# Kernel optimization log

Measured on AMD Instinct MI355X. Metric: run time of the kernel, lower is better.

The kernel has to match this reference:

```python
import jax, jax.numpy as jnp
import numpy as np

E = 512   # embed_size == hidden_size (required: step-0 'embed' is the init output of size hidden)
H = 512
A = 512   # attention dim
V = 20000
P = 196
B = 128
T = 24


def setup_inputs() -> dict:
    key = jax.random.key(0)
    ks = jax.random.split(key, 20)
    s = 0.02
    return {
        "features": jax.random.normal(ks[0], (B, P, E), jnp.float32),
        "captions": jax.random.randint(ks[1], (B, T), 0, V),
        "emb": jax.random.normal(ks[2], (V, E), jnp.float32) * s,
        "W_init_h": jax.random.normal(ks[3], (E, H), jnp.float32) * s,
        "b_init_h": jnp.zeros((H,), jnp.float32),
        "W_init_o": jax.random.normal(ks[4], (E, H), jnp.float32) * s,
        "b_init_o": jnp.zeros((H,), jnp.float32),
        "Wf": jax.random.normal(ks[5], (E, A), jnp.float32) * s,
        "bf": jnp.zeros((A,), jnp.float32),
        "Wh": jax.random.normal(ks[6], (H, A), jnp.float32) * s,
        "bh": jnp.zeros((A,), jnp.float32),
        "v_att": jax.random.normal(ks[7], (A,), jnp.float32) * s,
        "W_ih": jax.random.normal(ks[8], (3 * H, 2 * E), jnp.float32) * s,
        "W_hh": jax.random.normal(ks[9], (3 * H, H), jnp.float32) * s,
        "b_ih": jnp.zeros((3 * H,), jnp.float32),
        "b_hh": jnp.zeros((3 * H,), jnp.float32),
        "W_out": jax.random.normal(ks[10], (V, H), jnp.float32) * s,
        "b_out": jnp.zeros((V,), jnp.float32),
    }


def reference(features, emb, W_init_h, b_init_h, W_init_o, b_init_o,
              Wf, bf, Wh, bh, v_att, W_ih, W_hh, b_ih, b_hh,
              W_out, b_out, captions):
    # init_hidden_state
    avg = features.mean(axis=1)                          # [B,E]
    hidden0 = jnp.tanh(avg @ W_init_h + b_init_h)        # [B,H]
    output0 = jnp.tanh(avg @ W_init_o + b_init_o)        # [B,H]

    emb_caps = emb[captions]                             # [B,T,E]
    # teacher forcing: step 0 uses init output, step i>0 uses embeddings[:, i-1]
    embed_seq = jnp.concatenate([output0[:, None, :], emb_caps[:, :-1, :]], axis=1)
    xs = embed_seq.transpose(1, 0, 2)                    # [T,B,E]

    feat_proj = features @ Wf + bf                       # [B,P,A] (precompute attn key proj)

    def step(h, x_emb):
        # additive attention over pixels
        score = jnp.tanh(feat_proj + (h @ Wh + bh)[:, None, :]) @ v_att   # [B,P]
        alpha = jax.nn.softmax(score, axis=1)
        ctx = jnp.einsum('bp,bpe->be', alpha, features)                   # [B,E]
        x = jnp.concatenate([x_emb, ctx], axis=1)                         # [B,2E]
        # single-step GRU (PyTorch gate order r,z,n)
        gi = x @ W_ih.T + b_ih
        gh = h @ W_hh.T + b_hh
        gi_r, gi_z, gi_n = jnp.split(gi, 3, axis=1)
        gh_r, gh_z, gh_n = jnp.split(gh, 3, axis=1)
        r = jax.nn.sigmoid(gi_r + gh_r)
        z = jax.nn.sigmoid(gi_z + gh_z)
        n = jnp.tanh(gi_n + r * gh_n)
        h_new = (1.0 - z) * n + z * h
        pred = h_new @ W_out.T + b_out                                    # [B,V]
        return h_new, pred

    _, preds = jax.lax.scan(step, hidden0, xs)           # preds: [T,B,V]
    return preds.transpose(1, 0, 2)                      # [B,T,V]
```

## Files before the change

### kernel.cpp

```cpp
#include <hip/hip_runtime.h>

#define Bb 128
#define Tt 24
#define Ee 512
#define Hh 512
#define Aa 512
#define Vv 20000
#define Pp 196
#define TV (Tt*Vv)
#define NBLK 512
#define NTHR 256
#define GT (NBLK*NTHR)
#define SMEM_BYTES 34816

typedef __attribute__((ext_vector_type(8))) short bfrag;
typedef __attribute__((ext_vector_type(4))) float f4;
typedef __attribute__((ext_vector_type(4))) unsigned short us4;

#define MFMA16(a,b,c) __builtin_amdgcn_mfma_f32_16x16x32_bf16(a,b,c,0,0,0)

__device__ __forceinline__ unsigned short f2bf(float f){
  unsigned int x = __builtin_bit_cast(unsigned int, f);
  x += 0x7fffu + ((x >> 16) & 1u);
  return (unsigned short)(x >> 16);
}
__device__ __forceinline__ float bfu2f(unsigned short u){
  unsigned int x = ((unsigned int)u) << 16;
  return __builtin_bit_cast(float, x);
}
#define LOG2E 1.442695041f
__device__ __forceinline__ float fexp2(float x){ return __builtin_amdgcn_exp2f(x); }
__device__ __forceinline__ float frcp (float x){ return __builtin_amdgcn_rcpf(x); }
__device__ __forceinline__ float tanh_f(float x){ return 1.0f - 2.0f*frcp(1.0f + fexp2((2.0f*LOG2E)*x)); }
__device__ __forceinline__ float sigm_f(float x){ return frcp(1.0f + fexp2(-LOG2E*x)); }

__device__ __forceinline__ unsigned long long scld8(const void* p){
  return __hip_atomic_load((const unsigned long long*)p, __ATOMIC_RELAXED, __HIP_MEMORY_SCOPE_AGENT);
}
__device__ __forceinline__ unsigned scld4(const unsigned* p){
  return __hip_atomic_load(p, __ATOMIC_RELAXED, __HIP_MEMORY_SCOPE_AGENT);
}
__device__ __forceinline__ void scst4(unsigned* p, unsigned v){
  __hip_atomic_store(p, v, __ATOMIC_RELAXED, __HIP_MEMORY_SCOPE_AGENT);
}
__device__ __forceinline__ void scstf(float* p, float v){
  __hip_atomic_store(p, v, __ATOMIC_RELAXED, __HIP_MEMORY_SCOPE_AGENT);
}

__device__ __forceinline__ void set_flag(unsigned* line, unsigned v){
  asm volatile("s_waitcnt vmcnt(0)" ::: "memory");
  __syncthreads();
  if(threadIdx.x == 0) scst4(line, v);
}
__device__ __forceinline__ void poll_flags(const unsigned* base, int n, unsigned tgt){
  int tid = threadIdx.x;
  for(;;){
    int ok = (tid < n) ? (scld4(base + tid*16) >= tgt) : 1;
    if(__syncthreads_count(ok) == NTHR) break;
    __builtin_amdgcn_s_sleep(4);
  }
  asm volatile("" ::: "memory");
}

__device__ __forceinline__ void gbar2(unsigned* sync, unsigned phase){
  __syncthreads();
  int tid = threadIdx.x, blk = blockIdx.x;
  if(tid == 0)
    (void)__hip_atomic_fetch_add(sync + (blk & 31)*16, 1u,
                                 __ATOMIC_RELEASE, __HIP_MEMORY_SCOPE_AGENT);
  if(blk == 0){
    for(;;){
      int ok = (tid < 32) ? (scld4(sync + tid*16) >= phase*16u) : 1;
      if(__syncthreads_count(ok) == NTHR) break;
      __builtin_amdgcn_s_sleep(2);
    }
    if(tid == 0) scst4(sync + 32*16, phase);
  }
  if(tid == 0){
    while(scld4(sync + 32*16) < phase) __builtin_amdgcn_s_sleep(2);
    (void)__hip_atomic_load(sync + 32*16, __ATOMIC_ACQUIRE, __HIP_MEMORY_SCOPE_AGENT);
  }
  __syncthreads();
}

__global__ void k_zero(unsigned* s){
  int i = blockIdx.x*256 + threadIdx.x;
  s[i] = 0u;
}

__device__ __forceinline__ void cast_loop(const float* __restrict__ s,
                                          unsigned short* __restrict__ d,
                                          int n4, int gtid){
  for(int i = gtid; i < n4; i += GT){
    float4 v = ((const float4*)s)[i];
    us4 o; o[0]=f2bf(v.x); o[1]=f2bf(v.y); o[2]=f2bf(v.z); o[3]=f2bf(v.w);
    ((us4*)d)[i] = o;
  }
}
__device__ __forceinline__ void tr_tile(const float* __restrict__ S,
                                        unsigned short* __restrict__ D,
                                        int it, int jt, int tid, float (*T)[33]){
  int er = tid>>3, c4 = (tid&7)*4;
  float4 v = *(const float4*)(S + (size_t)(jt*32+er)*512 + it*32 + c4);
  T[er][c4+0]=v.x; T[er][c4+1]=v.y; T[er][c4+2]=v.z; T[er][c4+3]=v.w;
  __syncthreads();
  us4 o;
  o[0]=f2bf(T[c4+0][er]); o[1]=f2bf(T[c4+1][er]);
  o[2]=f2bf(T[c4+2][er]); o[3]=f2bf(T[c4+3][er]);
  *(us4*)(D + (size_t)(it*32+er)*512 + jt*32 + c4) = o;
  __syncthreads();
}

__device__ __forceinline__ void stage16(char* dstSM, const unsigned short* src, int R0){
  int tid = threadIdx.x;
  #pragma unroll
  for(int j=0;j<8;j++){
    int u = tid + j*256;
    int row = u >> 7, c8 = u & 127;
    unsigned long long q = scld8(src + (size_t)(R0+row)*Hh + c8*4);
    int bo = (row<<10) + (c8<<3);
    bo ^= (row&7)<<4;
    *(unsigned long long*)(dstSM + bo) = q;
  }
}


__device__ void attention_task(int b, const float* __restrict__ hpr_t,
                               const unsigned short* __restrict__ fpb,
                               const unsigned short* __restrict__ featsB,
                               const float* __restrict__ vatt,
                               unsigned short* __restrict__ ctx_t, char* SM)
{
  float* hp  = (float*)SM;
  float* vp  = hp + 512;
  float* sc  = vp + 512;
  float* red = sc + 200;
  int tid = threadIdx.x;
  {
    unsigned long long q = scld8(hpr_t + (size_t)b*Aa + tid*2);
    float2 hv = __builtin_bit_cast(float2, q);
    float2 vv = *(const float2*)(vatt + tid*2);
    int a0 = tid*2, a1 = a0+1;
    hp[((a0&31)<<4)+(a0>>5)] = hv.x;
    hp[((a1&31)<<4)+(a1>>5)] = hv.y;
    vp[((a0&31)<<4)+(a0>>5)] = vv.x;
    vp[((a1&31)<<4)+(a1>>5)] = vv.y;
  }
  __syncthreads();
  int grp = tid >> 4, gl = tid & 15;
  for(int pass=0; pass<13; pass++){
    int p = pass*16 + grp;
    float acc = 0.0f;
    if(p < Pp){
      const unsigned short* fr = fpb + ((size_t)b*Pp + p)*Aa + gl*32;
      #pragma unroll
      for(int j=0;j<32;j+=8){
        bfrag fv = *(const bfrag*)(fr + j);
        #pragma unroll
        for(int q=0;q<8;q++){
          int idx = ((j+q)<<4) + gl;
          float x = bfu2f((unsigned short)fv[q]) + hp[idx];
          acc += tanh_f(x) * vp[idx];
        }
      }
    }
    acc += __shfl_xor(acc, 1, 64);
    acc += __shfl_xor(acc, 2, 64);
    acc += __shfl_xor(acc, 4, 64);
    acc += __shfl_xor(acc, 8, 64);
    if(p < Pp && gl == 0) sc[p] = acc;
  }
  __syncthreads();
  if(tid < 64){
    float m = -1e30f;
    for(int i=0;i<4;i++){ int p = tid + i*64; if(p < Pp) m = fmaxf(m, sc[p]); }
    for(int off=1; off<64; off<<=1) m = fmaxf(m, __shfl_xor(m, off, 64));
    float s = 0.0f;
    for(int i=0;i<4;i++){ int p = tid + i*64; if(p < Pp) s += fexp2((sc[p]-m)*LOG2E); }
    for(int off=1; off<64; off<<=1) s += __shfl_xor(s, off, 64);
    if(tid == 0){ red[0] = m; red[1] = frcp(s); }
  }
  __syncthreads();
  float mx = red[0], rS = red[1];
  float al_t = 0.0f;
  if(tid < Pp) al_t = fexp2((sc[tid]-mx)*LOG2E) * rS;
  __syncthreads();
  if(tid < Pp) sc[tid] = al_t;
  __syncthreads();
  float c0 = 0.f, c1 = 0.f;
  const unsigned int* fb = (const unsigned int*)(featsB + (size_t)b*Pp*Ee);
  for(int p=0;p<Pp;p++){
    float al = sc[p];
    unsigned int u = fb[(size_t)p*256 + tid];
    unsigned int lo = (u & 0xffffu) << 16, hi = u & 0xffff0000u;
    c0 += al * __builtin_bit_cast(float, lo);
    c1 += al * __builtin_bit_cast(float, hi);
  }
  unsigned int cw = ((unsigned int)f2bf(c1) << 16) | (unsigned int)f2bf(c0);
  scst4((unsigned*)ctx_t + (size_t)b*256 + tid, cw);
}

__device__ void hproj_mfma(int R0, int HC0, const char* SMh,
                           const unsigned short* __restrict__ WhT,
                           const float* __restrict__ bhv, float* __restrict__ hpr)
{
  int tid = threadIdx.x;
  int w = tid>>6, l = tid&63, l16 = l&15, lk = l>>4;
  int a = HC0 + w*16 + l16;
  f4 acc = (f4)(0.0f);
  for(int k0=0;k0<512;k0+=32){
    int koff = k0 + lk*8;
    int bo = (l16<<10) + (koff<<1); bo ^= (l16&7)<<4;
    bfrag ah = *(const bfrag*)(SMh + bo);
    bfrag bq = *(const bfrag*)(WhT + (size_t)a*Hh + koff);
    acc = MFMA16(ah, bq, acc);
  }
  float bias = bhv[a];
  #pragma unroll
  for(int i=0;i<4;i++){
    int row = lk*4 + i;
    scstf(hpr + (size_t)(R0+row)*Aa + a, acc[i] + bias);
  }
}

__device__ void gates_phaseA(int R0, int HC0, const unsigned short* __restrict__ eseqT,
                             const unsigned short* __restrict__ WihB,
                             const unsigned short* __restrict__ WhhB,
                             const char* SMh, f4 (&agh)[3], f4 (&agi)[3])
{
  int tid = threadIdx.x;
  int w = tid>>6, l = tid&63, l16 = l&15, lk = l>>4;
  int hcol = HC0 + w*16 + l16;
  #pragma unroll
  for(int q=0;q<3;q++){ agh[q]=(f4)(0.f); agi[q]=(f4)(0.f); }
  for(int k0=0;k0<512;k0+=32){
    int koff = k0 + lk*8;
    int bo = (l16<<10) + (koff<<1); bo ^= (l16&7)<<4;
    bfrag ah = *(const bfrag*)(SMh + bo);
    bfrag ae = *(const bfrag*)(eseqT + (size_t)(R0+l16)*Ee + koff);
    #pragma unroll
    for(int q=0;q<3;q++){
      int j = q*512 + hcol;
      bfrag bh_ = *(const bfrag*)(WhhB + (size_t)j*512  + koff);
      bfrag be  = *(const bfrag*)(WihB + (size_t)j*1024 + koff);
      agh[q] = MFMA16(ah, bh_, agh[q]);
      agi[q] = MFMA16(ae, be,  agi[q]);
    }
  }
}

__device__ void gates_phaseB(int R0, int HC0, const char* SMc,
                             const unsigned short* __restrict__ WihB,
                             const float* __restrict__ bih, const float* __restrict__ bhh,
                             const float* __restrict__ hf_cur, float* __restrict__ hf_nxt,
                             unsigned short* __restrict__ hbU_nxt,
                             f4 (&agh)[3], f4 (&agi)[3], char* SM_HB)
{
  int tid = threadIdx.x;
  int w = tid>>6, l = tid&63, l16 = l&15, lk = l>>4;
  int hcol = HC0 + w*16 + l16;
  for(int k0=0;k0<512;k0+=32){
    int koff = k0 + lk*8;
    int bo = (l16<<10) + (koff<<1); bo ^= (l16&7)<<4;
    bfrag ac = *(const bfrag*)(SMc + bo);
    #pragma unroll
    for(int q=0;q<3;q++){
      int j = q*512 + hcol;
      bfrag bc = *(const bfrag*)(WihB + (size_t)j*1024 + 512 + koff);
      agi[q] = MFMA16(ac, bc, agi[q]);
    }
  }
  float bir = bih[hcol],      bhr = bhh[hcol];
  float biz = bih[512+hcol],  bhz = bhh[512+hcol];
  float bin = bih[1024+hcol], bhn = bhh[1024+hcol];
  unsigned short (*HB)[64] = (unsigned short(*)[64])SM_HB;
  #pragma unroll
  for(int i=0;i<4;i++){
    int row = lk*4 + i;
    int b = R0 + row;
    float r_ = sigm_f(agi[0][i] + bir + agh[0][i] + bhr);
    float z_ = sigm_f(agi[1][i] + biz + agh[1][i] + bhz);
    float n_ = tanh_f(agi[2][i] + bin + r_*(agh[2][i] + bhn));
    float ho = hf_cur[(size_t)b*Hh + hcol];
    float hn = (1.0f - z_)*n_ + z_*ho;
    hf_nxt[(size_t)b*Hh + hcol] = hn;
    HB[row][w*16 + l16] = f2bf(hn);
  }
  __syncthreads();
  #pragma unroll
  for(int j=0;j<2;j++){
    int widx = tid + j*256;
    int row = widx >> 5, pr = widx & 31;
    unsigned uu = (unsigned)HB[row][pr*2] | ((unsigned)HB[row][pr*2+1] << 16);
    scst4((unsigned*)(hbU_nxt + (size_t)(R0+row)*Hh + HC0) + pr, uu);
  }
}

__device__ void pred_task32(int pt, int tw, const unsigned short* __restrict__ hb_cur,
                            const unsigned short* __restrict__ WoutB,
                            const float* __restrict__ bout, float* __restrict__ out,
                            char* SM)
{
  int tid = threadIdx.x;
  int vchunk = pt >> 2, mbase = (pt & 3)*32;
  #pragma unroll
  for(int j=0;j<16;j++){
    int u = tid + j*256;
    int row = u >> 7, c8 = u & 127;
    unsigned long long q = scld8(hb_cur + (size_t)(mbase+row)*Hh + c8*4);
    int bo = (row<<10) + (c8<<3);
    bo ^= (row&7)<<4;
    *(unsigned long long*)(SM + bo) = q;
  }
  __syncthreads();
  int w = tid>>6, l = tid&63, l16 = l&15, lk = l>>4;
  int nb = vchunk*256 + w*64;
  f4 acc[2][4];
  #pragma unroll
  for(int mi=0;mi<2;mi++) for(int ni=0;ni<4;ni++) acc[mi][ni] = (f4)(0.0f);
  for(int k0=0;k0<512;k0+=32){
    int koff = k0 + lk*8;
    bfrag af[2], bq[4];
    #pragma unroll
    for(int mi=0;mi<2;mi++){
      int row = mi*16 + l16;
      int bo = (row<<10) + (koff<<1);
      bo ^= (row&7)<<4;
      af[mi] = *(const bfrag*)(SM + bo);
    }
    #pragma unroll
    for(int ni=0;ni<4;ni++){
      int v = nb + ni*16 + l16; if(v > Vv-1) v = Vv-1;
      bq[ni] = *(const bfrag*)(WoutB + (size_t)v*Hh + koff);
    }
    #pragma unroll
    for(int mi=0;mi<2;mi++)
      #pragma unroll
      for(int ni=0;ni<4;ni++)
        acc[mi][ni] = MFMA16(af[mi], bq[ni], acc[mi][ni]);
  }
  #pragma unroll
  for(int ni=0;ni<4;ni++){
    int v = nb + ni*16 + l16;
    if(v < Vv){
      float bias = bout[v];
      #pragma unroll
      for(int mi=0;mi<2;mi++){
        #pragma unroll
        for(int i=0;i<4;i++){
          int br = mbase + mi*16 + lk*4 + i;
          __builtin_nontemporal_store(acc[mi][ni][i] + bias,
              out + (size_t)br*TV + (size_t)tw*Vv + v);
        }
      }
    }
  }
  __syncthreads();
}

__global__ __launch_bounds__(NTHR, 4) void k_all(
    const float* feats, const int* caps, const float* emb,
    const float* Winh, const float* binh, const float* Wino, const float* bino,
    const float* Wf, const float* bfv, const float* Wh, const float* bhv,
    const float* vatt, const float* Wih, const float* Whh,
    const float* bih, const float* bhh, const float* Wout, const float* bout,
    float* out,
    float* hfR, unsigned short* hbU, float* hpr,
    unsigned short* ctxR, unsigned short* avgB, unsigned short* eseq,
    unsigned short* WfT, unsigned short* WhT,
    unsigned short* WinhT, unsigned short* WinoT,
    unsigned short* WihB, unsigned short* WhhB,
    unsigned short* fpb, unsigned short* featsB, unsigned short* WoutB,
    unsigned* sync)
{
  extern __shared__ char SMEM[];
  const int blk = blockIdx.x, tid = threadIdx.x;
  const int gtid = blk*NTHR + tid;
  unsigned* flagsA = sync + 40*16;
  unsigned* flagsG = sync + 168*16;
  unsigned* flagsP = sync + 240*16;
  unsigned* aggP   = sync + 304*16;
  float* h_f0 = hfR;
  unsigned short* h_b0 = hbU;

  cast_loop(Wih,  WihB,  (3*Hh*2*Ee)/4, gtid);
  cast_loop(Whh,  WhhB,  (3*Hh*Hh)/4,   gtid);
  cast_loop(Wout, WoutB, (Vv*Hh)/4,     gtid);
  cast_loop(feats,featsB,(Bb*Pp*Ee)/4,  gtid);
  for(int task = blk; task < 1024; task += NBLK){
    int z = task >> 8, rt = task & 255;
    int it = rt & 15, jt = rt >> 4;
    const float* S = (z==0)?Wf:(z==1)?Wh:(z==2)?Winh:Wino;
    unsigned short* D = (z==0)?WfT:(z==1)?WhT:(z==2)?WinhT:WinoT;
    tr_tile(S, D, it, jt, tid, (float(*)[33])SMEM);
  }
  if(blk < Bb){
    int b = blk;
    const float* fb = feats + (size_t)b*Pp*Ee;
    float a0=0.f, a1=0.f;
    for(int p=0;p<Pp;p++){
      float2 v = *(const float2*)(fb + (size_t)p*Ee + tid*2);
      a0 += v.x; a1 += v.y;
    }
    a0 *= (1.0f/Pp); a1 *= (1.0f/Pp);
    unsigned int pack = ((unsigned int)f2bf(a1)<<16) | (unsigned int)f2bf(a0);
    ((unsigned int*)avgB)[(size_t)b*256 + tid] = pack;
  }
  for(int task = blk; task < (Tt-1)*Bb; task += NBLK){
    int ts = task/Bb + 1, b = task%Bb;
    int cap = caps[b*Tt + (ts-1)];
    float2 v = *(const float2*)(emb + (size_t)cap*Ee + tid*2);
    unsigned int pack = ((unsigned int)f2bf(v.y)<<16) | (unsigned int)f2bf(v.x);
    ((unsigned int*)(eseq + ((size_t)ts*Bb + b)*Ee))[tid] = pack;
  }
  gbar2(sync, 1);

  for(int task = blk; task < 1584; task += NBLK){
    int w = tid>>6, l = tid&63, l16 = l&15, lk = l>>4;
    if(task < 1568){
      int bx = task % 196, by = task / 196;
      size_t m_base = (size_t)bx*128 + (w&1)*64;
      int nb = by*64 + (w>>1)*32;
      f4 acc[4][2];
      #pragma unroll
      for(int mi=0;mi<4;mi++) for(int ni=0;ni<2;ni++) acc[mi][ni] = (f4)(0.0f);
      for(int k0=0;k0<512;k0+=32){
        int koff = k0 + lk*8;
        bfrag af[4], bq[2];
        #pragma unroll
        for(int mi=0;mi<4;mi++) af[mi] = *(const bfrag*)(featsB + (m_base+mi*16+l16)*512 + koff);
        #pragma unroll
        for(int ni=0;ni<2;ni++) bq[ni] = *(const bfrag*)(WfT + (size_t)(nb+ni*16+l16)*512 + koff);
        #pragma unroll
        for(int mi=0;mi<4;mi++)
          #pragma unroll
          for(int ni=0;ni<2;ni++)
            acc[mi][ni] = MFMA16(af[mi], bq[ni], acc[mi][ni]);
      }
      #pragma unroll
      for(int ni=0;ni<2;ni++){
        int a = nb + ni*16 + l16;
        float bias = bfv[a];
        #pragma unroll
        for(int mi=0;mi<4;mi++){
          size_t r = m_base + mi*16 + lk*4;
          #pragma unroll
          for(int i=0;i<4;i++)
            fpb[(r+i)*512 + a] = f2bf(acc[mi][ni][i] + bias);
        }
      }
    } else {
      int idx = task - 1568;
      int y = idx >> 3, xb = idx & 7;
      int m0 = (w&1)*64, nb = xb*64 + (w>>1)*32;
      const unsigned short* Wt = y ? WinoT : WinhT;
      const float* bias = y ? bino : binh;
      f4 acc[4][2];
      #pragma unroll
      for(int mi=0;mi<4;mi++) for(int ni=0;ni<2;ni++) acc[mi][ni] = (f4)(0.0f);
      for(int k0=0;k0<512;k0+=32){
        int koff = k0 + lk*8;
        bfrag af[4], bq[2];
        #pragma unroll
        for(int mi=0;mi<4;mi++) af[mi] = *(const bfrag*)(avgB + (size_t)(m0+mi*16+l16)*512 + koff);
        #pragma unroll
        for(int ni=0;ni<2;ni++) bq[ni] = *(const bfrag*)(Wt + (size_t)(nb+ni*16+l16)*512 + koff);
        #pragma unroll
        for(int mi=0;mi<4;mi++)
          #pragma unroll
          for(int ni=0;ni<2;ni++)
            acc[mi][ni] = MFMA16(af[mi], bq[ni], acc[mi][ni]);
      }
      #pragma unroll
      for(int ni=0;ni<2;ni++){
        int n = nb + ni*16 + l16;
        float bv = bias[n];
        #pragma unroll
        for(int mi=0;mi<4;mi++){
          int bb = m0 + mi*16 + lk*4;
          #pragma unroll
          for(int i=0;i<4;i++){
            float val = tanh_f(acc[mi][ni][i] + bv);
            if(y==0){ h_f0[(size_t)(bb+i)*Hh + n] = val; h_b0[(size_t)(bb+i)*Hh + n] = f2bf(val); }
            else    { eseq[(size_t)(bb+i)*Ee + n] = f2bf(val); }
          }
        }
      }
    }
  }
  gbar2(sync, 2);

  int xcd = blk & 7, slot = blk >> 3;

  if(slot < 16){
    int b = slot*8 + xcd;
    int rg = b >> 4;
    for(int t=0; t<Tt; t++){
      poll_flags(flagsP + rg*8*16, 8, (unsigned)(t+1));
      attention_task(b, hpr + (size_t)(t&1)*Bb*Aa, fpb, featsB, vatt,
                     ctxR + (size_t)(t&3)*Bb*Ee, SMEM);
      set_flag(flagsA + b*16, (unsigned)(t+1));
    }
  } else if(slot < 24){
    int r = slot - 16, c = xcd;
    int R0 = r*16, HC0 = c*64;
    char* SMh = SMEM;
    char* SMc = SMEM + 16384;
    char* SMB = SMEM + 32768;
    f4 agh[3], agi[3];
    stage16(SMh, hbU, R0);
    __syncthreads();
    hproj_mfma(R0, HC0, SMh, WhT, bhv, hpr);
    set_flag(flagsP + (r*8+c)*16, 1u);
    gates_phaseA(R0, HC0, eseq, WihB, WhhB, SMh, agh, agi);
    for(int t=0; t<Tt; t++){
      poll_flags(flagsA + R0*16, 16, (unsigned)(t+1));
      stage16(SMc, ctxR + (size_t)(t&3)*Bb*Ee, R0);
      __syncthreads();
      gates_phaseB(R0, HC0, SMc, WihB, bih, bhh,
                   hfR + (size_t)(t&1)*Bb*Hh, hfR + (size_t)((t+1)&1)*Bb*Hh,
                   hbU + (size_t)(t+1)*Bb*Hh, agh, agi, SMB);
      set_flag(flagsG + (r*8+c)*16, (unsigned)(t+1));
      if(t+1 < Tt){
        poll_flags(flagsG + r*8*16, 8, (unsigned)(t+1));
        stage16(SMh, hbU + (size_t)(t+1)*Bb*Hh, R0);
        __syncthreads();
        hproj_mfma(R0, HC0, SMh, WhT, bhv, hpr + (size_t)((t+1)&1)*Bb*Aa);
        set_flag(flagsP + (r*8+c)*16, (unsigned)(t+2));
        gates_phaseA(R0, HC0, eseq + (size_t)(t+1)*Bb*Ee, WihB, WhhB, SMh, agh, agi);
      }
    }
  } else {
    int ps = slot - 24;
    int pt = xcd*40 + ps;
    if(ps == 0){
      for(int t=1; t<=Tt; t++){
        poll_flags(flagsG, 64, (unsigned)t);
        if(tid == 0) scst4(aggP + xcd*16, (unsigned)t);
        pred_task32(pt, t-1, hbU + (size_t)t*Bb*Hh, WoutB, bout, out, SMEM);
      }
    } else if(pt < 316){
      for(int t=1; t<=Tt; t++){
        poll_flags(aggP + xcd*16, 1, (unsigned)t);
        pred_task32(pt, t-1, hbU + (size_t)t*Bb*Hh, WoutB, bout, out, SMEM);
      }
    }
  }
}

extern "C" void kernel_launch(void* const* d_in, const int* in_sizes, int n_in,
                              void* d_out, int out_size, void* d_ws, size_t ws_size,
                              hipStream_t stream)
{
  const float* feats = (const float*)d_in[0];
  const int*   caps  = (const int*)d_in[1];
  const float* emb   = (const float*)d_in[2];
  const float* Winh  = (const float*)d_in[3];
  const float* binh  = (const float*)d_in[4];
  const float* Wino  = (const float*)d_in[5];
  const float* bino  = (const float*)d_in[6];
  const float* Wf    = (const float*)d_in[7];
  const float* bfv   = (const float*)d_in[8];
  const float* Wh    = (const float*)d_in[9];
  const float* bhv   = (const float*)d_in[10];
  const float* vatt  = (const float*)d_in[11];
  const float* Wih   = (const float*)d_in[12];
  const float* Whh   = (const float*)d_in[13];
  const float* bih   = (const float*)d_in[14];
  const float* bhh   = (const float*)d_in[15];
  const float* Wout  = (const float*)d_in[16];
  const float* bout  = (const float*)d_in[17];
  float* out = (float*)d_out;

  char* ws = (char*)d_ws;
  size_t off = 0;
  auto alloc = [&](size_t bytes){
    off = (off + 255) & ~(size_t)255;
    void* p = ws + off; off += bytes; return p;
  };
  unsigned* syncp = (unsigned*)alloc(32768);
  float* hfR = (float*)alloc((size_t)2*Bb*Hh*4);
  unsigned short* hbU = (unsigned short*)alloc((size_t)(Tt+1)*Bb*Hh*2);
  float* hpr = (float*)alloc((size_t)2*Bb*Aa*4);
  unsigned short* ctxR  = (unsigned short*)alloc((size_t)4*Bb*Ee*2);
  unsigned short* avgB  = (unsigned short*)alloc((size_t)Bb*Ee*2);
  unsigned short* eseq  = (unsigned short*)alloc((size_t)Tt*Bb*Ee*2);
  unsigned short* WfT   = (unsigned short*)alloc((size_t)Ee*Aa*2);
  unsigned short* WhT   = (unsigned short*)alloc((size_t)Hh*Aa*2);
  unsigned short* WinhT = (unsigned short*)alloc((size_t)Ee*Hh*2);
  unsigned short* WinoT = (unsigned short*)alloc((size_t)Ee*Hh*2);
  unsigned short* WihB  = (unsigned short*)alloc((size_t)3*Hh*2*Ee*2);
  unsigned short* WhhB  = (unsigned short*)alloc((size_t)3*Hh*Hh*2);
  unsigned short* fpb   = (unsigned short*)alloc((size_t)Bb*Pp*Aa*2);
  unsigned short* featsB= (unsigned short*)alloc((size_t)Bb*Pp*Ee*2);
  unsigned short* WoutB = (unsigned short*)alloc((size_t)Vv*Hh*2);
  if(ws_size < off) return;

  k_zero<<<32, 256, 0, stream>>>(syncp);
  k_all<<<NBLK, NTHR, SMEM_BYTES, stream>>>(
      feats, caps, emb, Winh, binh, Wino, bino, Wf, bfv, Wh, bhv, vatt,
      Wih, Whh, bih, bhh, Wout, bout, out,
      hfR, hbU, hpr, ctxR, avgB, eseq,
      WfT, WhT, WinhT, WinoT, WihB, WhhB, fpb, featsB, WoutB, syncp);
}
```

Before: 1.445 ms.

## Compute split-K hidden projection partials from local GRU output before barrier

Result: slower. 1.786 ms (+23.6%).

```diff
diff --git a/kernel.cpp b/kernel.cpp
--- a/kernel.cpp
+++ b/kernel.cpp
@@ -11,7 +11,7 @@
 #define NBLK 512
 #define NTHR 256
 #define GT (NBLK*NTHR)
-#define SMEM_BYTES 34816
+#define SMEM_BYTES 35584
 
 typedef __attribute__((ext_vector_type(8))) short bfrag;
 typedef __attribute__((ext_vector_type(4))) float f4;
@@ -57,7 +57,7 @@
   for(;;){
     int ok = (tid < n) ? (scld4(base + tid*16) >= tgt) : 1;
     if(__syncthreads_count(ok) == NTHR) break;
-    __builtin_amdgcn_s_sleep(4);
+    __builtin_amdgcn_s_sleep(2);
   }
   asm volatile("" ::: "memory");
 }
@@ -125,7 +125,8 @@
 }
 
 
-__device__ void attention_task(int b, const float* __restrict__ hpr_t,
+__device__ void attention_task(int b, const float* __restrict__ hprP,
+                               const float* __restrict__ bhv,
                                const unsigned short* __restrict__ fpb,
                                const unsigned short* __restrict__ featsB,
                                const float* __restrict__ vatt,
@@ -137,12 +138,17 @@
   float* red = sc + 200;
   int tid = threadIdx.x;
   {
-    unsigned long long q = scld8(hpr_t + (size_t)b*Aa + tid*2);
-    float2 hv = __builtin_bit_cast(float2, q);
-    float2 vv = *(const float2*)(vatt + tid*2);
     int a0 = tid*2, a1 = a0+1;
-    hp[((a0&31)<<4)+(a0>>5)] = hv.x;
-    hp[((a1&31)<<4)+(a1>>5)] = hv.y;
+    float s0 = bhv[a0], s1 = bhv[a1];
+    #pragma unroll
+    for(int c=0;c<8;c++){
+      unsigned long long q = scld8(hprP + ((size_t)c*Bb + b)*Aa + a0);
+      float2 pv = __builtin_bit_cast(float2, q);
+      s0 += pv.x; s1 += pv.y;
+    }
+    float2 vv = *(const float2*)(vatt + a0);
+    hp[((a0&31)<<4)+(a0>>5)] = s0;
+    hp[((a1&31)<<4)+(a1>>5)] = s1;
     vp[((a0&31)<<4)+(a0>>5)] = vv.x;
     vp[((a1&31)<<4)+(a1>>5)] = vv.y;
   }
@@ -189,6 +195,7 @@
   __syncthreads();
   float c0 = 0.f, c1 = 0.f;
   const unsigned int* fb = (const unsigned int*)(featsB + (size_t)b*Pp*Ee);
+  #pragma unroll 4
   for(int p=0;p<Pp;p++){
     float al = sc[p];
     unsigned int u = fb[(size_t)p*256 + tid];
@@ -200,26 +207,45 @@
   scst4((unsigned*)ctx_t + (size_t)b*256 + tid, cw);
 }
 
-__device__ void hproj_mfma(int R0, int HC0, const char* SMh,
+__device__ void hprojP_SMh(int R0, int HC0, const char* SMh,
                            const unsigned short* __restrict__ WhT,
-                           const float* __restrict__ bhv, float* __restrict__ hpr)
-{
-  int tid = threadIdx.x;
-  int w = tid>>6, l = tid&63, l16 = l&15, lk = l>>4;
-  int a = HC0 + w*16 + l16;
-  f4 acc = (f4)(0.0f);
-  for(int k0=0;k0<512;k0+=32){
-    int koff = k0 + lk*8;
-    int bo = (l16<<10) + (koff<<1); bo ^= (l16&7)<<4;
-    bfrag ah = *(const bfrag*)(SMh + bo);
-    bfrag bq = *(const bfrag*)(WhT + (size_t)a*Hh + koff);
-    acc = MFMA16(ah, bq, acc);
-  }
-  float bias = bhv[a];
-  #pragma unroll
-  for(int i=0;i<4;i++){
-    int row = lk*4 + i;
-    scstf(hpr + (size_t)(R0+row)*Aa + a, acc[i] + bias);
+                           float* __restrict__ hprPc)
+{
+  int tid = threadIdx.x, w = tid>>6, l = tid&63, l16 = l&15, lk = l>>4;
+  for(int nt=0; nt<8; nt++){
+    int a = (w*8+nt)*16 + l16;
+    f4 acc = (f4)(0.0f);
+    #pragma unroll
+    for(int kk=0; kk<2; kk++){
+      int col = HC0 + kk*32 + lk*8;
+      int bo = (l16<<10) + (col<<1); bo ^= (l16&7)<<4;
+      bfrag af = *(const bfrag*)(SMh + bo);
+      bfrag bq = *(const bfrag*)(WhT + (size_t)a*Hh + col);
+      acc = MFMA16(af, bq, acc);
+    }
+    #pragma unroll
+    for(int i=0;i<4;i++)
+      scstf(hprPc + (size_t)(R0 + lk*4 + i)*Aa + a, acc[i]);
+  }
+}
+
+__device__ void hprojP_HB(int R0, int HC0, const unsigned short* HBp,
+                          const unsigned short* __restrict__ WhT,
+                          float* __restrict__ hprPc)
+{
+  int tid = threadIdx.x, w = tid>>6, l = tid&63, l16 = l&15, lk = l>>4;
+  for(int nt=0; nt<8; nt++){
+    int a = (w*8+nt)*16 + l16;
+    f4 acc = (f4)(0.0f);
+    #pragma unroll
+    for(int kk=0; kk<2; kk++){
+      bfrag af = *(const bfrag*)(HBp + l16*88 + kk*32 + lk*8);
+      bfrag bq = *(const bfrag*)(WhT + (size_t)a*Hh + HC0 + kk*32 + lk*8);
+      acc = MFMA16(af, bq, acc);
+    }
+    #pragma unroll
+    for(int i=0;i<4;i++)
+      scstf(hprPc + (size_t)(R0 + lk*4 + i)*Aa + a, acc[i]);
   }
 }
 
@@ -254,7 +280,7 @@
                              const float* __restrict__ bih, const float* __restrict__ bhh,
                              const float* __restrict__ hf_cur, float* __restrict__ hf_nxt,
                              unsigned short* __restrict__ hbU_nxt,
-                             f4 (&agh)[3], f4 (&agi)[3], char* SM_HB)
+                             f4 (&agh)[3], f4 (&agi)[3], unsigned short* HBp)
 {
   int tid = threadIdx.x;
   int w = tid>>6, l = tid&63, l16 = l&15, lk = l>>4;
@@ -273,7 +299,6 @@
   float bir = bih[hcol],      bhr = bhh[hcol];
   float biz = bih[512+hcol],  bhz = bhh[512+hcol];
   float bin = bih[1024+hcol], bhn = bhh[1024+hcol];
-  unsigned short (*HB)[64] = (unsigned short(*)[64])SM_HB;
   #pragma unroll
   for(int i=0;i<4;i++){
     int row = lk*4 + i;
@@ -284,14 +309,14 @@
     float ho = hf_cur[(size_t)b*Hh + hcol];
     float hn = (1.0f - z_)*n_ + z_*ho;
     hf_nxt[(size_t)b*Hh + hcol] = hn;
-    HB[row][w*16 + l16] = f2bf(hn);
+    HBp[row*88 + w*16 + l16] = f2bf(hn);
   }
   __syncthreads();
   #pragma unroll
   for(int j=0;j<2;j++){
     int widx = tid + j*256;
     int row = widx >> 5, pr = widx & 31;
-    unsigned uu = (unsigned)HB[row][pr*2] | ((unsigned)HB[row][pr*2+1] << 16);
+    unsigned uu = (unsigned)HBp[row*88 + pr*2] | ((unsigned)HBp[row*88 + pr*2+1] << 16);
     scst4((unsigned*)(hbU_nxt + (size_t)(R0+row)*Hh + HC0) + pr, uu);
   }
 }
@@ -365,7 +390,7 @@
     const float* vatt, const float* Wih, const float* Whh,
     const float* bih, const float* bhh, const float* Wout, const float* bout,
     float* out,
-    float* hfR, unsigned short* hbU, float* hpr,
+    float* hfR, unsigned short* hbU, float* hprP,
     unsigned short* ctxR, unsigned short* avgB, unsigned short* eseq,
     unsigned short* WfT, unsigned short* WhT,
     unsigned short* WinhT, unsigned short* WinoT,
@@ -497,7 +522,7 @@
     int rg = b >> 4;
     for(int t=0; t<Tt; t++){
       poll_flags(flagsP + rg*8*16, 8, (unsigned)(t+1));
-      attention_task(b, hpr + (size_t)(t&1)*Bb*Aa, fpb, featsB, vatt,
+      attention_task(b, hprP, bhv, fpb, featsB, vatt,
                      ctxR + (size_t)(t&3)*Bb*Ee, SMEM);
       set_flag(flagsA + b*16, (unsigned)(t+1));
     }
@@ -506,11 +531,12 @@
     int R0 = r*16, HC0 = c*64;
     char* SMh = SMEM;
     char* SMc = SMEM + 16384;
-    char* SMB = SMEM + 32768;
+    unsigned short* HBp = (unsigned short*)(SMEM + 32768);
+    float* hprPc = hprP + (size_t)c*Bb*Aa;
     f4 agh[3], agi[3];
     stage16(SMh, hbU, R0);
     __syncthreads();
-    hproj_mfma(R0, HC0, SMh, WhT, bhv, hpr);
+    hprojP_SMh(R0, HC0, SMh, WhT, hprPc);
     set_flag(flagsP + (r*8+c)*16, 1u);
     gates_phaseA(R0, HC0, eseq, WihB, WhhB, SMh, agh, agi);
     for(int t=0; t<Tt; t++){
@@ -519,15 +545,17 @@
       __syncthreads();
       gates_phaseB(R0, HC0, SMc, WihB, bih, bhh,
                    hfR + (size_t)(t&1)*Bb*Hh, hfR + (size_t)((t+1)&1)*Bb*Hh,
-                   hbU + (size_t)(t+1)*Bb*Hh, agh, agi, SMB);
-      set_flag(flagsG + (r*8+c)*16, (unsigned)(t+1));
+                   hbU + (size_t)(t+1)*Bb*Hh, agh, agi, HBp);
       if(t+1 < Tt){
+        hprojP_HB(R0, HC0, HBp, WhT, hprPc);
+        set_flag(flagsP + (r*8+c)*16, (unsigned)(t+2));
+        set_flag(flagsG + (r*8+c)*16, (unsigned)(t+1));
         poll_flags(flagsG + r*8*16, 8, (unsigned)(t+1));
         stage16(SMh, hbU + (size_t)(t+1)*Bb*Hh, R0);
         __syncthreads();
-        hproj_mfma(R0, HC0, SMh, WhT, bhv, hpr + (size_t)((t+1)&1)*Bb*Aa);
-        set_flag(flagsP + (r*8+c)*16, (unsigned)(t+2));
         gates_phaseA(R0, HC0, eseq + (size_t)(t+1)*Bb*Ee, WihB, WhhB, SMh, agh, agi);
+      } else {
+        set_flag(flagsG + (r*8+c)*16, (unsigned)(t+1));
       }
     }
   } else {
@@ -581,7 +609,7 @@
   unsigned* syncp = (unsigned*)alloc(32768);
   float* hfR = (float*)alloc((size_t)2*Bb*Hh*4);
   unsigned short* hbU = (unsigned short*)alloc((size_t)(Tt+1)*Bb*Hh*2);
-  float* hpr = (float*)alloc((size_t)2*Bb*Aa*4);
+  float* hprP = (float*)alloc((size_t)8*Bb*Aa*4);
   unsigned short* ctxR  = (unsigned short*)alloc((size_t)4*Bb*Ee*2);
   unsigned short* avgB  = (unsigned short*)alloc((size_t)Bb*Ee*2);
   unsigned short* eseq  = (unsigned short*)alloc((size_t)Tt*Bb*Ee*2);
@@ -600,6 +628,6 @@
   k_all<<<NBLK, NTHR, SMEM_BYTES, stream>>>(
       feats, caps, emb, Winh, binh, Wino, bino, Wf, bfv, Wh, bhv, vatt,
       Wih, Whh, bih, bhh, Wout, bout, out,
-      hfR, hbU, hpr, ctxR, avgB, eseq,
+      hfR, hbU, hprP, ctxR, avgB, eseq,
       WfT, WhT, WinhT, WinoT, WihB, WhhB, fpb, featsB, WoutB, syncp);
 }
```

## Split attention across all blocks with partial softmax and grid barriers per phase

Applied to the files above, without the earlier changes.

Result: slower. 2.348 ms (+62.5%).

```diff
diff --git a/kernel.cpp b/kernel.cpp
--- a/kernel.cpp
+++ b/kernel.cpp
@@ -11,7 +11,7 @@
 #define NBLK 512
 #define NTHR 256
 #define GT (NBLK*NTHR)
-#define SMEM_BYTES 34816
+#define LEADER 480
 
 typedef __attribute__((ext_vector_type(8))) short bfrag;
 typedef __attribute__((ext_vector_type(4))) float f4;
@@ -46,19 +46,29 @@
 __device__ __forceinline__ void scstf(float* p, float v){
   __hip_atomic_store(p, v, __ATOMIC_RELAXED, __HIP_MEMORY_SCOPE_AGENT);
 }
-
-__device__ __forceinline__ void set_flag(unsigned* line, unsigned v){
+__device__ __forceinline__ void scst8(void* p, unsigned long long v){
+  __hip_atomic_store((unsigned long long*)p, v, __ATOMIC_RELAXED, __HIP_MEMORY_SCOPE_AGENT);
+}
+
+__device__ __forceinline__ void sbar(unsigned* sync, unsigned k){
   asm volatile("s_waitcnt vmcnt(0)" ::: "memory");
   __syncthreads();
-  if(threadIdx.x == 0) scst4(line, v);
-}
-__device__ __forceinline__ void poll_flags(const unsigned* base, int n, unsigned tgt){
-  int tid = threadIdx.x;
-  for(;;){
-    int ok = (tid < n) ? (scld4(base + tid*16) >= tgt) : 1;
-    if(__syncthreads_count(ok) == NTHR) break;
-    __builtin_amdgcn_s_sleep(4);
-  }
+  int tid = threadIdx.x;
+  if(tid == 0)
+    (void)__hip_atomic_fetch_add(sync + (blockIdx.x & 31)*16, 1u,
+                                 __ATOMIC_RELAXED, __HIP_MEMORY_SCOPE_AGENT);
+  if(blockIdx.x == LEADER){
+    for(;;){
+      int ok = (tid < 32) ? (scld4(sync + tid*16) >= k*16u) : 1;
+      if(__syncthreads_count(ok) == NTHR) break;
+      __builtin_amdgcn_s_sleep(2);
+    }
+    if(tid == 0) scst4(sync + 32*16, k);
+  }
+  if(tid == 0){
+    while(scld4(sync + 32*16) < k) __builtin_amdgcn_s_sleep(2);
+  }
+  __syncthreads();
   asm volatile("" ::: "memory");
 }
 
@@ -125,19 +135,19 @@
 }
 
 
-__device__ void attention_task(int b, const float* __restrict__ hpr_t,
-                               const unsigned short* __restrict__ fpb,
-                               const unsigned short* __restrict__ featsB,
-                               const float* __restrict__ vatt,
-                               unsigned short* __restrict__ ctx_t, char* SM)
-{
-  float* hp  = (float*)SM;
-  float* vp  = hp + 512;
-  float* sc  = vp + 512;
-  float* red = sc + 200;
+__device__ void attn_sub(int b, int j, const float* __restrict__ hpr,
+                         const unsigned short* __restrict__ fpb,
+                         const unsigned short* __restrict__ featsB,
+                         const float* __restrict__ vatt,
+                         float* __restrict__ cpartP, float* __restrict__ msP,
+                         char* SM)
+{
+  float* hp = (float*)SM;
+  float* vp = hp + 512;
+  float* sc = vp + 512;
   int tid = threadIdx.x;
   {
-    unsigned long long q = scld8(hpr_t + (size_t)b*Aa + tid*2);
+    unsigned long long q = scld8(hpr + (size_t)b*Aa + tid*2);
     float2 hv = __builtin_bit_cast(float2, q);
     float2 vv = *(const float2*)(vatt + tid*2);
     int a0 = tid*2, a1 = a0+1;
@@ -148,17 +158,18 @@
   }
   __syncthreads();
   int grp = tid >> 4, gl = tid & 15;
-  for(int pass=0; pass<13; pass++){
-    int p = pass*16 + grp;
+  int pbase = j*49;
+  for(int pass=0; pass<4; pass++){
+    int lp = pass*16 + grp;
     float acc = 0.0f;
-    if(p < Pp){
-      const unsigned short* fr = fpb + ((size_t)b*Pp + p)*Aa + gl*32;
+    if(lp < 49){
+      const unsigned short* fr = fpb + ((size_t)b*Pp + pbase + lp)*Aa + gl*32;
       #pragma unroll
-      for(int j=0;j<32;j+=8){
-        bfrag fv = *(const bfrag*)(fr + j);
+      for(int jj=0;jj<32;jj+=8){
+        bfrag fv = *(const bfrag*)(fr + jj);
         #pragma unroll
         for(int q=0;q<8;q++){
-          int idx = ((j+q)<<4) + gl;
+          int idx = ((jj+q)<<4) + gl;
           float x = bfu2f((unsigned short)fv[q]) + hp[idx];
           acc += tanh_f(x) * vp[idx];
         }
@@ -168,36 +179,75 @@
     acc += __shfl_xor(acc, 2, 64);
     acc += __shfl_xor(acc, 4, 64);
     acc += __shfl_xor(acc, 8, 64);
-    if(p < Pp && gl == 0) sc[p] = acc;
+    if(lp < 49 && gl == 0) sc[lp] = acc;
   }
   __syncthreads();
   if(tid < 64){
-    float m = -1e30f;
-    for(int i=0;i<4;i++){ int p = tid + i*64; if(p < Pp) m = fmaxf(m, sc[p]); }
+    float v = (tid < 49) ? sc[tid] : -1e30f;
+    float m = v;
     for(int off=1; off<64; off<<=1) m = fmaxf(m, __shfl_xor(m, off, 64));
-    float s = 0.0f;
-    for(int i=0;i<4;i++){ int p = tid + i*64; if(p < Pp) s += fexp2((sc[p]-m)*LOG2E); }
+    float e = (tid < 49) ? fexp2((sc[tid]-m)*LOG2E) : 0.0f;
+    if(tid < 49) sc[tid] = e;
+    float s = e;
     for(int off=1; off<64; off<<=1) s += __shfl_xor(s, off, 64);
-    if(tid == 0){ red[0] = m; red[1] = frcp(s); }
-  }
-  __syncthreads();
-  float mx = red[0], rS = red[1];
-  float al_t = 0.0f;
-  if(tid < Pp) al_t = fexp2((sc[tid]-mx)*LOG2E) * rS;
-  __syncthreads();
-  if(tid < Pp) sc[tid] = al_t;
-  __syncthreads();
+    if(tid == 0){
+      float2 ms; ms.x = m; ms.y = s;
+      scst8(msP + ((size_t)j*Bb + b)*2, __builtin_bit_cast(unsigned long long, ms));
+    }
+  }
+  __syncthreads();
+  int cc = tid*2;
   float c0 = 0.f, c1 = 0.f;
-  const unsigned int* fb = (const unsigned int*)(featsB + (size_t)b*Pp*Ee);
-  for(int p=0;p<Pp;p++){
-    float al = sc[p];
-    unsigned int u = fb[(size_t)p*256 + tid];
+  const unsigned int* fb = (const unsigned int*)(featsB + ((size_t)b*Pp + pbase)*Ee);
+  for(int lp=0; lp<49; lp++){
+    float al = sc[lp];
+    unsigned int u = fb[(size_t)lp*256 + tid];
     unsigned int lo = (u & 0xffffu) << 16, hi = u & 0xffff0000u;
     c0 += al * __builtin_bit_cast(float, lo);
     c1 += al * __builtin_bit_cast(float, hi);
   }
-  unsigned int cw = ((unsigned int)f2bf(c1) << 16) | (unsigned int)f2bf(c0);
-  scst4((unsigned*)ctx_t + (size_t)b*256 + tid, cw);
+  float2 cp; cp.x = c0; cp.y = c1;
+  scst8(cpartP + ((size_t)j*Bb + b)*Ee + cc, __builtin_bit_cast(unsigned long long, cp));
+}
+
+__device__ void gates_combine_stage(int R0, const float* __restrict__ cpartP,
+                                    const float* __restrict__ msP,
+                                    char* SMc, float* wv)
+{
+  int tid = threadIdx.x;
+  if(tid < 16){
+    int row = R0 + tid;
+    float m[4], s[4];
+    #pragma unroll
+    for(int j=0;j<4;j++){
+      unsigned long long q = scld8(msP + ((size_t)j*Bb + row)*2);
+      float2 ms = __builtin_bit_cast(float2, q);
+      m[j] = ms.x; s[j] = ms.y;
+    }
+    float M = fmaxf(fmaxf(m[0],m[1]), fmaxf(m[2],m[3]));
+    float S = 0.f; float w[4];
+    #pragma unroll
+    for(int j=0;j<4;j++){ w[j] = fexp2((m[j]-M)*LOG2E); S += w[j]*s[j]; }
+    float rS = frcp(S);
+    #pragma unroll
+    for(int j=0;j<4;j++) wv[tid*4+j] = w[j]*rS;
+  }
+  __syncthreads();
+  int cc = tid*2;
+  #pragma unroll 4
+  for(int rr=0; rr<16; rr++){
+    float a0 = 0.f, a1 = 0.f;
+    #pragma unroll
+    for(int j=0;j<4;j++){
+      unsigned long long q = scld8(cpartP + ((size_t)j*Bb + R0+rr)*Ee + cc);
+      float2 cp = __builtin_bit_cast(float2, q);
+      float w = wv[rr*4+j];
+      a0 += w*cp.x; a1 += w*cp.y;
+    }
+    unsigned pk = ((unsigned)f2bf(a1) << 16) | (unsigned)f2bf(a0);
+    int bo = (rr<<10) + (cc<<1); bo ^= (rr&7)<<4;
+    *(unsigned*)(SMc + bo) = pk;
+  }
 }
 
 __device__ void hproj_mfma(int R0, int HC0, const char* SMh,
@@ -240,9 +290,9 @@
     bfrag ae = *(const bfrag*)(eseqT + (size_t)(R0+l16)*Ee + koff);
     #pragma unroll
     for(int q=0;q<3;q++){
-      int j = q*512 + hcol;
-      bfrag bh_ = *(const bfrag*)(WhhB + (size_t)j*512  + koff);
-      bfrag be  = *(const bfrag*)(WihB + (size_t)j*1024 + koff);
+      int jj = q*512 + hcol;
+      bfrag bh_ = *(const bfrag*)(WhhB + (size_t)jj*512  + koff);
+      bfrag be  = *(const bfrag*)(WihB + (size_t)jj*1024 + koff);
       agh[q] = MFMA16(ah, bh_, agh[q]);
       agi[q] = MFMA16(ae, be,  agi[q]);
     }
@@ -254,7 +304,7 @@
                              const float* __restrict__ bih, const float* __restrict__ bhh,
                              const float* __restrict__ hf_cur, float* __restrict__ hf_nxt,
                              unsigned short* __restrict__ hbU_nxt,
-                             f4 (&agh)[3], f4 (&agi)[3], char* SM_HB)
+                             f4 (&agh)[3], f4 (&agi)[3], unsigned short* HBp)
 {
   int tid = threadIdx.x;
   int w = tid>>6, l = tid&63, l16 = l&15, lk = l>>4;
@@ -265,15 +315,14 @@
     bfrag ac = *(const bfrag*)(SMc + bo);
     #pragma unroll
     for(int q=0;q<3;q++){
-      int j = q*512 + hcol;
-      bfrag bc = *(const bfrag*)(WihB + (size_t)j*1024 + 512 + koff);
+      int jj = q*512 + hcol;
+      bfrag bc = *(const bfrag*)(WihB + (size_t)jj*1024 + 512 + koff);
       agi[q] = MFMA16(ac, bc, agi[q]);
     }
   }
   float bir = bih[hcol],      bhr = bhh[hcol];
   float biz = bih[512+hcol],  bhz = bhh[512+hcol];
   float bin = bih[1024+hcol], bhn = bhh[1024+hcol];
-  unsigned short (*HB)[64] = (unsigned short(*)[64])SM_HB;
   #pragma unroll
   for(int i=0;i<4;i++){
     int row = lk*4 + i;
@@ -284,14 +333,14 @@
     float ho = hf_cur[(size_t)b*Hh + hcol];
     float hn = (1.0f - z_)*n_ + z_*ho;
     hf_nxt[(size_t)b*Hh + hcol] = hn;
-    HB[row][w*16 + l16] = f2bf(hn);
+    HBp[row*88 + w*16 + l16] = f2bf(hn);
   }
   __syncthreads();
   #pragma unroll
   for(int j=0;j<2;j++){
     int widx = tid + j*256;
     int row = widx >> 5, pr = widx & 31;
-    unsigned uu = (unsigned)HB[row][pr*2] | ((unsigned)HB[row][pr*2+1] << 16);
+    unsigned uu = (unsigned)HBp[row*88 + pr*2] | ((unsigned)HBp[row*88 + pr*2+1] << 16);
     scst4((unsigned*)(hbU_nxt + (size_t)(R0+row)*Hh + HC0) + pr, uu);
   }
 }
@@ -358,28 +407,24 @@
   __syncthreads();
 }
 
-__global__ __launch_bounds__(NTHR, 4) void k_all(
+__global__ __launch_bounds__(NTHR, 2) void k_all(
     const float* feats, const int* caps, const float* emb,
     const float* Winh, const float* binh, const float* Wino, const float* bino,
     const float* Wf, const float* bfv, const float* Wh, const float* bhv,
     const float* vatt, const float* Wih, const float* Whh,
     const float* bih, const float* bhh, const float* Wout, const float* bout,
     float* out,
-    float* hfR, unsigned short* hbU, float* hpr,
-    unsigned short* ctxR, unsigned short* avgB, unsigned short* eseq,
+    float* hfR, unsigned short* hbU, float* hpr, float* cpartP, float* msP,
+    unsigned short* avgB, unsigned short* eseq,
     unsigned short* WfT, unsigned short* WhT,
     unsigned short* WinhT, unsigned short* WinoT,
     unsigned short* WihB, unsigned short* WhhB,
     unsigned short* fpb, unsigned short* featsB, unsigned short* WoutB,
     unsigned* sync)
 {
-  extern __shared__ char SMEM[];
+  __shared__ char SMEM[33792];
   const int blk = blockIdx.x, tid = threadIdx.x;
   const int gtid = blk*NTHR + tid;
-  unsigned* flagsA = sync + 40*16;
-  unsigned* flagsG = sync + 168*16;
-  unsigned* flagsP = sync + 240*16;
-  unsigned* aggP   = sync + 304*16;
   float* h_f0 = hfR;
   unsigned short* h_b0 = hbU;
 
@@ -490,61 +535,61 @@
   }
   gbar2(sync, 2);
 
-  int xcd = blk & 7, slot = blk >> 3;
-
-  if(slot < 16){
-    int b = slot*8 + xcd;
-    int rg = b >> 4;
-    for(int t=0; t<Tt; t++){
-      poll_flags(flagsP + rg*8*16, 8, (unsigned)(t+1));
-      attention_task(b, hpr + (size_t)(t&1)*Bb*Aa, fpb, featsB, vatt,
-                     ctxR + (size_t)(t&3)*Bb*Ee, SMEM);
-      set_flag(flagsA + b*16, (unsigned)(t+1));
-    }
-  } else if(slot < 24){
-    int r = slot - 16, c = xcd;
-    int R0 = r*16, HC0 = c*64;
-    char* SMh = SMEM;
-    char* SMc = SMEM + 16384;
-    char* SMB = SMEM + 32768;
-    f4 agh[3], agi[3];
-    stage16(SMh, hbU, R0);
+  int role_b = blk & 127, role_j = blk >> 7;
+  bool isGates = (blk < 64);
+  bool isHproj = (blk >= 64 && blk < 128);
+  bool isPred  = (blk >= 64 && blk < 380);
+  int gr = blk >> 3, gc = blk & 7;
+  int hid = blk - 64;
+  int hr = hid >> 3, hc = hid & 7;
+  int pid = blk - 64;
+  int xcd_p = pid & 7, slot_p = pid >> 3;
+  int pt = (xcd_p < 4) ? (xcd_p*40 + slot_p) : (160 + (xcd_p-4)*39 + slot_p);
+  unsigned bk = 3;
+  f4 agh[3], agi[3];
+  char* SMc = SMEM;
+  float* WS = (float*)(SMEM + 16384);
+  unsigned short* HBp = (unsigned short*)(SMEM + 16384 + 256);
+
+  if(isGates){
+    stage16(SMEM, hbU, gr*16);
     __syncthreads();
-    hproj_mfma(R0, HC0, SMh, WhT, bhv, hpr);
-    set_flag(flagsP + (r*8+c)*16, 1u);
-    gates_phaseA(R0, HC0, eseq, WihB, WhhB, SMh, agh, agi);
-    for(int t=0; t<Tt; t++){
-      poll_flags(flagsA + R0*16, 16, (unsigned)(t+1));
-      stage16(SMc, ctxR + (size_t)(t&3)*Bb*Ee, R0);
+    gates_phaseA(gr*16, gc*64, eseq, WihB, WhhB, SMEM, agh, agi);
+  } else if(isHproj){
+    stage16(SMEM, hbU, hr*16);
+    __syncthreads();
+    hproj_mfma(hr*16, hc*64, SMEM, WhT, bhv, hpr);
+  }
+  sbar(sync, bk++);
+
+  for(int t=0; t<Tt; t++){
+    attn_sub(role_b, role_j, hpr, fpb, featsB, vatt, cpartP, msP, SMEM);
+    sbar(sync, bk++);
+    if(isGates){
+      gates_combine_stage(gr*16, cpartP, msP, SMc, WS);
       __syncthreads();
-      gates_phaseB(R0, HC0, SMc, WihB, bih, bhh,
+      gates_phaseB(gr*16, gc*64, SMc, WihB, bih, bhh,
                    hfR + (size_t)(t&1)*Bb*Hh, hfR + (size_t)((t+1)&1)*Bb*Hh,
-                   hbU + (size_t)(t+1)*Bb*Hh, agh, agi, SMB);
-      set_flag(flagsG + (r*8+c)*16, (unsigned)(t+1));
-      if(t+1 < Tt){
-        poll_flags(flagsG + r*8*16, 8, (unsigned)(t+1));
-        stage16(SMh, hbU + (size_t)(t+1)*Bb*Hh, R0);
+                   hbU + (size_t)(t+1)*Bb*Hh, agh, agi, HBp);
+    } else if(isPred && t >= 1 && pt < 316){
+      pred_task32(pt, t-1, hbU + (size_t)t*Bb*Hh, WoutB, bout, out, SMEM);
+    }
+    sbar(sync, bk++);
+    if(t < Tt-1){
+      if(isGates){
+        stage16(SMEM, hbU + (size_t)(t+1)*Bb*Hh, gr*16);
         __syncthreads();
-        hproj_mfma(R0, HC0, SMh, WhT, bhv, hpr + (size_t)((t+1)&1)*Bb*Aa);
-        set_flag(flagsP + (r*8+c)*16, (unsigned)(t+2));
-        gates_phaseA(R0, HC0, eseq + (size_t)(t+1)*Bb*Ee, WihB, WhhB, SMh, agh, agi);
+        gates_phaseA(gr*16, gc*64, eseq + (size_t)(t+1)*Bb*Ee, WihB, WhhB, SMEM, agh, agi);
+      } else if(isHproj){
+        stage16(SMEM, hbU + (size_t)(t+1)*Bb*Hh, hr*16);
+        __syncthreads();
+        hproj_mfma(hr*16, hc*64, SMEM, WhT, bhv, hpr);
       }
-    }
-  } else {
-    int ps = slot - 24;
-    int pt = xcd*40 + ps;
-    if(ps == 0){
-      for(int t=1; t<=Tt; t++){
-        poll_flags(flagsG, 64, (unsigned)t);
-        if(tid == 0) scst4(aggP + xcd*16, (unsigned)t);
-        pred_task32(pt, t-1, hbU + (size_t)t*Bb*Hh, WoutB, bout, out, SMEM);
-      }
-    } else if(pt < 316){
-      for(int t=1; t<=Tt; t++){
-        poll_flags(aggP + xcd*16, 1, (unsigned)t);
-        pred_task32(pt, t-1, hbU + (size_t)t*Bb*Hh, WoutB, bout, out, SMEM);
-      }
-    }
+    } else {
+      if(isPred && pt < 316)
+        pred_task32(pt, Tt-1, hbU + (size_t)Tt*Bb*Hh, WoutB, bout, out, SMEM);
+    }
+    sbar(sync, bk++);
   }
 }
 
@@ -581,8 +626,9 @@
   unsigned* syncp = (unsigned*)alloc(32768);
   float* hfR = (float*)alloc((size_t)2*Bb*Hh*4);
   unsigned short* hbU = (unsigned short*)alloc((size_t)(Tt+1)*Bb*Hh*2);
-  float* hpr = (float*)alloc((size_t)2*Bb*Aa*4);
-  unsigned short* ctxR  = (unsigned short*)alloc((size_t)4*Bb*Ee*2);
+  float* hpr = (float*)alloc((size_t)Bb*Aa*4);
+  float* cpartP = (float*)alloc((size_t)4*Bb*Ee*4);
+  float* msP = (float*)alloc((size_t)4*Bb*2*4);
   unsigned short* avgB  = (unsigned short*)alloc((size_t)Bb*Ee*2);
   unsigned short* eseq  = (unsigned short*)alloc((size_t)Tt*Bb*Ee*2);
   unsigned short* WfT   = (unsigned short*)alloc((size_t)Ee*Aa*2);
@@ -597,9 +643,9 @@
   if(ws_size < off) return;
 
   k_zero<<<32, 256, 0, stream>>>(syncp);
-  k_all<<<NBLK, NTHR, SMEM_BYTES, stream>>>(
+  k_all<<<NBLK, NTHR, 0, stream>>>(
       feats, caps, emb, Winh, binh, Wino, bino, Wf, bfv, Wh, bhv, vatt,
       Wih, Whh, bih, bhh, Wout, bout, out,
-      hfR, hbU, hpr, ctxR, avgB, eseq,
+      hfR, hbU, hpr, cpartP, msP, avgB, eseq,
       WfT, WhT, WinhT, WinoT, WihB, WhhB, fpb, featsB, WoutB, syncp);
 }
```
